# Kernel tuning notes

Measured on AMD Instinct MI355X. Metric: run time of the kernel, lower is better.

## Reference

```python
import jax, jax.numpy as jnp
import numpy as np

V_REST = 0.0
V_RESET = 0.0
V_TH = 1.27
TAU = 50.0
SPIKE_DURATION = 1
SCALE = 100.0  # SurrGradSpike.scale


@jax.custom_vjp
def spike(x):
    return (x > 0).astype(x.dtype)

def _spike_fwd(x):
    return (x > 0).astype(x.dtype), x

def _spike_bwd(x, g):
    # normalized negative part of fast sigmoid (Zenke & Ganguli 2018)
    return (g / (SCALE * jnp.abs(x) + 1.0) ** 2,)

spike.defvjp(_spike_fwd, _spike_bwd)


def _shift(a, k):
    # a[:, j] -> a[:, j + k], zero padded out of range
    if k == 0:
        return a
    if k > 0:
        return jnp.pad(a[:, k:], ((0, 0), (0, k)))
    return jnp.pad(a[:, :k], ((0, 0), (-k, 0)))


def _lif(ode, decay):
    ode2 = ode[..., 0]          # [B, T]
    B, T = ode2.shape
    ode_t = ode2.T              # [T, B] for scan

    def step(carry, inp):
        v, counter, z = carry   # z = remaining steps whose dv reads are zeroed
        t, x = inp
        v = v - decay * (v - V_REST)
        v = jnp.where(counter == 1, V_RESET, v)
        # dv[:, t] was zeroed by a spike within the previous 5 steps (torch in-place window)
        x_eff = jnp.where(z > 0, 0.0, x)
        v = v + x_eff
        v = jnp.where(counter > 1, V_TH, v)
        s = spike(v - V_TH)
        s_d = jax.lax.stop_gradient(s)
        counter = counter + (SPIKE_DURATION + 1) * s_d
        v = jnp.where(counter > 1, V_TH, v)
        # spike at t zeroes dv[:, t-1:t+6]; at t==0 the torch slice [-1:6] is empty
        z = jnp.where((s_d > 0) & (t >= 1), 5.0, jnp.maximum(z - 1.0, 0.0))
        counter = jnp.maximum(counter - 1.0, 0.0)
        return (v, counter, z), (v, s, s_d)

    v0 = jnp.full((B,), V_REST, dtype=ode2.dtype)
    c0 = jnp.zeros((B,), dtype=ode2.dtype)
    z0 = jnp.zeros((B,), dtype=ode2.dtype)
    ts = jnp.arange(T)
    _, (v_rec, s_rec, sd_rec) = jax.lax.scan(step, (v0, c0, z0), (ts, ode_t))
    v_rec = v_rec.T             # [B, T]
    s_rec = s_rec.T             # [B, T]

    sp = sd_rec.T > 0           # detached spike mask [B, T]
    sp = sp.at[:, 0].set(False)  # spike at t=0 zeroes nothing (empty slice in torch)
    # column j of dv is zeroed iff a spike occurred at t' in [j-5, j+1]
    zero_mask = jnp.zeros_like(sp)
    for k in range(-5, 2):
        zero_mask = zero_mask | _shift(sp, k)
    dv = jnp.where(zero_mask, 0.0, ode2)
    return v_rec, s_rec, dv


def setup_inputs() -> dict:
    key = jax.random.key(0)
    B, T = 2048, 4096
    ode = jax.random.normal(key, (B, T, 1), dtype=jnp.float32)
    decay = jnp.float32(1.0 / TAU)  # LIF.decay parameter (learn_tau=False)
    return {"ode": ode, "decay": decay}


def reference(ode, decay):
    return _lif(ode, decay)
```

## Files before the change

kernel.cpp:

```cpp
#include <hip/hip_runtime.h>

constexpr int   T   = 4096;
constexpr float VTH = 1.27f;
constexpr int   K   = 32;
constexpr int   L   = T / K;
constexpr int   LG  = L / 4;
constexpr int   WG  = 160;

__device__ __forceinline__ bool sstep(float x, float decay, float& v, unsigned& h, bool& gate) {
    float t1 = __fmul_rn(decay, v);
    float vd = __fsub_rn(v, t1);
    float xe = gate ? 0.0f : x;
    float vn = __fadd_rn(vd, xe);
    bool  s  = vn > VTH;
    v = s ? 0.0f : vn;
    bool g4 = (h & 15u) != 0u;
    h = (h << 1) | (s ? 1u : 0u);
    gate = s || g4;
    return s;
}

__device__ __forceinline__ bool ostep(float x, float decay, float& v, unsigned& h, bool& gate,
                                      float& vo, float& so, float& dvo, float xprev) {
    float t1 = __fmul_rn(decay, v);
    float vd = __fsub_rn(v, t1);
    float xe = gate ? 0.0f : x;
    float vn = __fadd_rn(vd, xe);
    bool  s  = vn > VTH;
    vo = s ? VTH  : vn;
    so = s ? 1.0f : 0.0f;
    v  = s ? 0.0f : vn;
    bool z6 = s || ((h & 63u) != 0u);
    dvo = z6 ? 0.0f : xprev;
    bool g4 = (h & 15u) != 0u;
    h = (h << 1) | (s ? 1u : 0u);
    gate = s || g4;
    return s;
}

__device__ __forceinline__ void ogroup(float4 X, float decay, float& v, unsigned& h, bool& gate,
                                       float& xprev, float4& vo, float4& so,
                                       float& close, float& px, float& py, float& pz) {
    ostep(X.x, decay, v, h, gate, vo.x, so.x, close, xprev); xprev = X.x;
    ostep(X.y, decay, v, h, gate, vo.y, so.y, px,    xprev); xprev = X.y;
    ostep(X.z, decay, v, h, gate, vo.z, so.z, py,    xprev); xprev = X.z;
    ostep(X.w, decay, v, h, gate, vo.w, so.w, pz,    xprev); xprev = X.w;
}

__device__ __forceinline__ void quad_run(int q, const float4* __restrict__ x4, int g0f,
        float decay, float& v, unsigned& h, bool& gate, float& xprev,
        float4& Xa, float4& Xb, float4& Xc, float4& Xd,
        float4& D0, float4& D1, float4& D2, float4& D3,
        float4& P0, float4& P1, float4& P2, float4& P3,
        float4* __restrict__ v4, float4* __restrict__ s4, float4* __restrict__ d4) {
    float4 V0, V1, V2, V3, S0, S1, S2, S3;
    ogroup(Xa, decay, v, h, gate, xprev, V0, S0, P3.w, D0.x, D0.y, D0.z);
    Xa = x4[g0f + (4*q + 8 < LG ? 4*q + 8 : LG - 1)];
    d4[g0f + 4*q - 4] = P0; d4[g0f + 4*q - 3] = P1;
    d4[g0f + 4*q - 2] = P2; d4[g0f + 4*q - 1] = P3;
    ogroup(Xb, decay, v, h, gate, xprev, V1, S1, D0.w, D1.x, D1.y, D1.z);
    Xb = x4[g0f + (4*q + 9 < LG ? 4*q + 9 : LG - 1)];
    ogroup(Xc, decay, v, h, gate, xprev, V2, S2, D1.w, D2.x, D2.y, D2.z);
    Xc = x4[g0f + (4*q + 10 < LG ? 4*q + 10 : LG - 1)];
    ogroup(Xd, decay, v, h, gate, xprev, V3, S3, D2.w, D3.x, D3.y, D3.z);
    Xd = x4[g0f + (4*q + 11 < LG ? 4*q + 11 : LG - 1)];
    v4[g0f + 4*q] = V0; v4[g0f + 4*q + 1] = V1; v4[g0f + 4*q + 2] = V2; v4[g0f + 4*q + 3] = V3;
    s4[g0f + 4*q] = S0; s4[g0f + 4*q + 1] = S1; s4[g0f + 4*q + 2] = S2; s4[g0f + 4*q + 3] = S3;
}

__global__ __launch_bounds__(64, 1)
void lif_spec(const float* __restrict__ ode, const float* __restrict__ decay_p,
              float* __restrict__ vout, float* __restrict__ sout, float* __restrict__ dvout,
              float2* __restrict__ Sst, float2* __restrict__ Est, int B) {
    const int g = blockIdx.x * 64 + threadIdx.x;
    const int b = g % B;
    const int k = g / B;
    const float decay = decay_p[0];

    const size_t bt = (size_t)b * T;
    const float4* __restrict__ x4 = (const float4*)(ode + bt);
    float4* __restrict__ v4 = (float4*)(vout + bt);
    float4* __restrict__ s4 = (float4*)(sout + bt);
    float4* __restrict__ d4 = (float4*)(dvout + bt);

    const int g0f = k * LG;
    const int wg  = (k == 0) ? 0 : (k * LG < WG ? k * LG : WG);
    float v = 0.0f; unsigned h = 0u; bool gate = false;
    float xprev = 0.0f;

    if (wg > 0) {
        const float4* __restrict__ xw = x4 + (g0f - wg);
        const bool t0row = (g0f - wg == 0);
        float4 Q[16];
#pragma unroll
        for (int i = 0; i < 16; ++i) Q[i] = xw[i];
        for (int c = 0; c < wg; c += 16) {
#pragma unroll
            for (int i = 0; i < 16; ++i) {
                if (i == 0 && c == 0 && t0row) {
                    sstep(Q[0].x, decay, v, h, gate); h = 0u; gate = false;
                    sstep(Q[0].y, decay, v, h, gate);
                    sstep(Q[0].z, decay, v, h, gate);
                    sstep(Q[0].w, decay, v, h, gate);
                } else {
                    sstep(Q[i].x, decay, v, h, gate);
                    sstep(Q[i].y, decay, v, h, gate);
                    sstep(Q[i].z, decay, v, h, gate);
                    sstep(Q[i].w, decay, v, h, gate);
                }
                Q[i] = xw[c + i + 16];
            }
        }
        Sst[k * B + b] = make_float2(v, __uint_as_float(h & 127u));
    }

    float xla = (k < K - 1) ? ode[bt + (size_t)(k + 1) * L] : 0.0f;
    float4 A0 = x4[g0f],     A1 = x4[g0f + 1], A2 = x4[g0f + 2], A3 = x4[g0f + 3];
    float4 B0 = x4[g0f + 4], B1 = x4[g0f + 5], B2 = x4[g0f + 6], B3 = x4[g0f + 7];
    float4 DA0, DA1, DA2, DA3, DB0, DB1, DB2, DB3;

    {
        float4 V0, V1, V2, V3, S0, S1, S2, S3;
        if (k == 0) {
            float dvd;
            bool s0 = ostep(A0.x, decay, v, h, gate, V0.x, S0.x, dvd, xprev); xprev = A0.x;
            h = 0u; gate = false;
            bool s1 = ostep(A0.y, decay, v, h, gate, V0.y, S0.y, DA0.x, xprev); xprev = A0.y;
            ostep(A0.z, decay, v, h, gate, V0.z, S0.z, DA0.y, xprev); xprev = A0.z;
            ostep(A0.w, decay, v, h, gate, V0.w, S0.w, DA0.z, xprev); xprev = A0.w;
            if (s0 && s1) V0.z = VTH;
        } else {
            float cl;
            ogroup(A0, decay, v, h, gate, xprev, V0, S0, cl, DA0.x, DA0.y, DA0.z);
        }
        A0 = x4[g0f + 8];
        ogroup(A1, decay, v, h, gate, xprev, V1, S1, DA0.w, DA1.x, DA1.y, DA1.z); A1 = x4[g0f + 9];
        ogroup(A2, decay, v, h, gate, xprev, V2, S2, DA1.w, DA2.x, DA2.y, DA2.z); A2 = x4[g0f + 10];
        ogroup(A3, decay, v, h, gate, xprev, V3, S3, DA2.w, DA3.x, DA3.y, DA3.z); A3 = x4[g0f + 11];
        v4[g0f] = V0; v4[g0f + 1] = V1; v4[g0f + 2] = V2; v4[g0f + 3] = V3;
        s4[g0f] = S0; s4[g0f + 1] = S1; s4[g0f + 2] = S2; s4[g0f + 3] = S3;
    }

#define MQ(q, Xs, Dn, Pn) quad_run(q, x4, g0f, decay, v, h, gate, xprev, \
        Xs##0, Xs##1, Xs##2, Xs##3, Dn##0, Dn##1, Dn##2, Dn##3, \
        Pn##0, Pn##1, Pn##2, Pn##3, v4, s4, d4);
    MQ(1, B, DB, DA) MQ(2, A, DA, DB) MQ(3, B, DB, DA) MQ(4, A, DA, DB)
    MQ(5, B, DB, DA) MQ(6, A, DA, DB) MQ(7, B, DB, DA)
#undef MQ

    Est[k * B + b] = make_float2(v, __uint_as_float(h & 127u));

    if (k < K - 1) {
        float vo_, so_;
        ostep(xla, decay, v, h, gate, vo_, so_, DB3.w, xprev);
    } else {
        DB3.w = ((h & 63u) != 0u) ? 0.0f : xprev;
    }
    d4[g0f + LG - 4] = DB0; d4[g0f + LG - 3] = DB1;
    d4[g0f + LG - 2] = DB2; d4[g0f + LG - 1] = DB3;
}

__global__ __launch_bounds__(64, 1)
void lif_fix(const float* __restrict__ ode, const float* __restrict__ decay_p,
             float* __restrict__ vout, float* __restrict__ sout, float* __restrict__ dvout,
             const float2* __restrict__ Sst, const float2* __restrict__ Est, int B) {
    const int b = blockIdx.x * 64 + threadIdx.x;
    const float decay = decay_p[0];

    float2 E = Est[b];
    for (int k = 1; k < K; ++k) {
        float2 S = Sst[k * B + b];
        bool match = (S.x == E.x) && (__float_as_uint(S.y) == __float_as_uint(E.y));
        if (match) { E = Est[k * B + b]; continue; }

        const size_t bt = (size_t)b * T;
        const float4* __restrict__ x4 = (const float4*)(ode + bt);
        float4* __restrict__ v4 = (float4*)(vout + bt);
        float4* __restrict__ s4 = (float4*)(sout + bt);
        float4* __restrict__ d4 = (float4*)(dvout + bt);
        const int g0f = k * LG;

        float v = E.x; unsigned h = __float_as_uint(E.y);
        bool gate = (h & 31u) != 0u;
        float xprev = 0.0f;
        float4 pend;

        float4 Q0 = x4[g0f], Q1 = x4[g0f + 1], Q2 = x4[g0f + 2], Q3 = x4[g0f + 3];
        {
            float4 vo, so; float cl;
            ogroup(Q0, decay, v, h, gate, xprev, vo, so, cl, pend.x, pend.y, pend.z);
            v4[g0f] = vo; s4[g0f] = so;
            Q0 = x4[g0f + 4];
        }
#define FPROC(cc, Q) { float4 vo, so; float px, py, pz; \
            ogroup(Q, decay, v, h, gate, xprev, vo, so, pend.w, px, py, pz); \
            d4[g0f + (cc) - 1] = pend; \
            pend.x = px; pend.y = py; pend.z = pz; \
            v4[g0f + (cc)] = vo; s4[g0f + (cc)] = so; }
        FPROC(1, Q1) Q1 = x4[g0f + 5];
        FPROC(2, Q2) Q2 = x4[g0f + 6];
        FPROC(3, Q3) Q3 = x4[g0f + 7];
        for (int c0 = 4; c0 < LG; c0 += 4) {
            FPROC(c0,     Q0) Q0 = x4[g0f + (c0 + 4 < LG ? c0 + 4 : LG - 1)];
            FPROC(c0 + 1, Q1) Q1 = x4[g0f + (c0 + 5 < LG ? c0 + 5 : LG - 1)];
            FPROC(c0 + 2, Q2) Q2 = x4[g0f + (c0 + 6 < LG ? c0 + 6 : LG - 1)];
            FPROC(c0 + 3, Q3) Q3 = x4[g0f + (c0 + 7 < LG ? c0 + 7 : LG - 1)];
        }
#undef FPROC
        E = make_float2(v, __uint_as_float(h & 127u));
        if (k < K - 1) {
            float xla = ode[bt + (size_t)(k + 1) * L];
            float vo_, so_;
            ostep(xla, decay, v, h, gate, vo_, so_, pend.w, xprev);
        } else {
            pend.w = ((h & 63u) != 0u) ? 0.0f : xprev;
        }
        d4[g0f + LG - 1] = pend;
    }
}

extern "C" void kernel_launch(void* const* d_in, const int* in_sizes, int n_in,
                              void* d_out, int out_size, void* d_ws, size_t ws_size,
                              hipStream_t stream) {
    const float* ode   = (const float*)d_in[0];
    const float* decay = (const float*)d_in[1];
    float* out = (float*)d_out;

    const int BT = in_sizes[0];
    const int B  = BT / T;

    float* vout  = out;
    float* sout  = out + (size_t)BT;
    float* dvout = out + 2 * (size_t)BT;

    float2* Sst = (float2*)d_ws;
    float2* Est = Sst + (size_t)K * B;

    lif_spec<<<dim3((B * K) / 64), dim3(64), 0, stream>>>(ode, decay, vout, sout, dvout,
                                                          Sst, Est, B);
    lif_fix<<<dim3(B / 64), dim3(64), 0, stream>>>(ode, decay, vout, sout, dvout,
                                                   Sst, Est, B);
}
```

Baseline: 194.4 us.

## Stage spec-kernel outputs through LDS for coalesced row stores; prefetch fix states

The speculative LIF kernel now buffers each thread's v, spike and dv float4 outputs in shared memory. After each quad of groups a barrier runs, and threads cooperatively write 16-float contiguous chunks spanning 4 rows. This replaces the previous per-thread strided stores, where each lane wrote a different row, so stores become more coalesced. The cost is a barrier per quad and extra LDS traffic. The fix kernel also prefetches the next chunk's start and end states one iteration ahead to hide load latency in its sequential loop.

```diff
diff --git a/kernel.cpp b/kernel.cpp
--- a/kernel.cpp
+++ b/kernel.cpp
@@ -47,41 +47,23 @@
     ostep(X.w, decay, v, h, gate, vo.w, so.w, pz,    xprev); xprev = X.w;
 }
 
-__device__ __forceinline__ void quad_run(int q, const float4* __restrict__ x4, int g0f,
-        float decay, float& v, unsigned& h, bool& gate, float& xprev,
-        float4& Xa, float4& Xb, float4& Xc, float4& Xd,
-        float4& D0, float4& D1, float4& D2, float4& D3,
-        float4& P0, float4& P1, float4& P2, float4& P3,
-        float4* __restrict__ v4, float4* __restrict__ s4, float4* __restrict__ d4) {
-    float4 V0, V1, V2, V3, S0, S1, S2, S3;
-    ogroup(Xa, decay, v, h, gate, xprev, V0, S0, P3.w, D0.x, D0.y, D0.z);
-    Xa = x4[g0f + (4*q + 8 < LG ? 4*q + 8 : LG - 1)];
-    d4[g0f + 4*q - 4] = P0; d4[g0f + 4*q - 3] = P1;
-    d4[g0f + 4*q - 2] = P2; d4[g0f + 4*q - 1] = P3;
-    ogroup(Xb, decay, v, h, gate, xprev, V1, S1, D0.w, D1.x, D1.y, D1.z);
-    Xb = x4[g0f + (4*q + 9 < LG ? 4*q + 9 : LG - 1)];
-    ogroup(Xc, decay, v, h, gate, xprev, V2, S2, D1.w, D2.x, D2.y, D2.z);
-    Xc = x4[g0f + (4*q + 10 < LG ? 4*q + 10 : LG - 1)];
-    ogroup(Xd, decay, v, h, gate, xprev, V3, S3, D2.w, D3.x, D3.y, D3.z);
-    Xd = x4[g0f + (4*q + 11 < LG ? 4*q + 11 : LG - 1)];
-    v4[g0f + 4*q] = V0; v4[g0f + 4*q + 1] = V1; v4[g0f + 4*q + 2] = V2; v4[g0f + 4*q + 3] = V3;
-    s4[g0f + 4*q] = S0; s4[g0f + 4*q + 1] = S1; s4[g0f + 4*q + 2] = S2; s4[g0f + 4*q + 3] = S3;
-}
-
 __global__ __launch_bounds__(64, 1)
 void lif_spec(const float* __restrict__ ode, const float* __restrict__ decay_p,
               float* __restrict__ vout, float* __restrict__ sout, float* __restrict__ dvout,
               float2* __restrict__ Sst, float2* __restrict__ Est, int B) {
-    const int g = blockIdx.x * 64 + threadIdx.x;
-    const int b = g % B;
-    const int k = g / B;
+    __shared__ float4 tv[64 * 5];
+    __shared__ float4 ts[64 * 5];
+    __shared__ float4 td[2][64 * 5];
+
+    const int tid = threadIdx.x;
+    const int gg  = blockIdx.x * 64;
+    const int rb  = gg % B;
+    const int k   = gg / B;
+    const int b   = rb + tid;
     const float decay = decay_p[0];
 
     const size_t bt = (size_t)b * T;
     const float4* __restrict__ x4 = (const float4*)(ode + bt);
-    float4* __restrict__ v4 = (float4*)(vout + bt);
-    float4* __restrict__ s4 = (float4*)(sout + bt);
-    float4* __restrict__ d4 = (float4*)(dvout + bt);
 
     const int g0f = k * LG;
     const int wg  = (k == 0) ? 0 : (k * LG < WG ? k * LG : WG);
@@ -114,50 +96,91 @@
         Sst[k * B + b] = make_float2(v, __uint_as_float(h & 127u));
     }
 
+    int rowoff0 = (rb + (tid >> 2)) * T + k * L + (tid & 3) * 4;
+    const int wbase = tid * 5;
+    const int rbase = (tid >> 2) * 5 + (tid & 3);
+
     float xla = (k < K - 1) ? ode[bt + (size_t)(k + 1) * L] : 0.0f;
     float4 A0 = x4[g0f],     A1 = x4[g0f + 1], A2 = x4[g0f + 2], A3 = x4[g0f + 3];
     float4 B0 = x4[g0f + 4], B1 = x4[g0f + 5], B2 = x4[g0f + 6], B3 = x4[g0f + 7];
-    float4 DA0, DA1, DA2, DA3, DB0, DB1, DB2, DB3;
+    float4 Pd;
+
+#define OG(X, gidx) { float4 V_, S_; float cl_, p0_, p1_, p2_; \
+        ogroup(X, decay, v, h, gate, xprev, V_, S_, cl_, p0_, p1_, p2_); \
+        if ((gidx) > 0) { Pd.w = cl_; td[(((gidx)-1) >> 2) & 1][wbase + (((gidx)-1) & 3)] = Pd; } \
+        Pd.x = p0_; Pd.y = p1_; Pd.z = p2_; \
+        tv[wbase + ((gidx) & 3)] = V_; ts[wbase + ((gidx) & 3)] = S_; }
+
+#define FLUSH(q) { __syncthreads(); \
+        float4 Vv0 = tv[rbase], Vv1 = tv[rbase + 80], Vv2 = tv[rbase + 160], Vv3 = tv[rbase + 240]; \
+        float4 Ss0 = ts[rbase], Ss1 = ts[rbase + 80], Ss2 = ts[rbase + 160], Ss3 = ts[rbase + 240]; \
+        *(float4*)(vout + rowoff0 + (q)*16)            = Vv0; \
+        *(float4*)(vout + rowoff0 + 16*T + (q)*16)     = Vv1; \
+        *(float4*)(vout + rowoff0 + 32*T + (q)*16)     = Vv2; \
+        *(float4*)(vout + rowoff0 + 48*T + (q)*16)     = Vv3; \
+        *(float4*)(sout + rowoff0 + (q)*16)            = Ss0; \
+        *(float4*)(sout + rowoff0 + 16*T + (q)*16)     = Ss1; \
+        *(float4*)(sout + rowoff0 + 32*T + (q)*16)     = Ss2; \
+        *(float4*)(sout + rowoff0 + 48*T + (q)*16)     = Ss3; \
+        if ((q) >= 1) { \
+            float4 Dd0 = td[((q)-1)&1][rbase],       Dd1 = td[((q)-1)&1][rbase + 80]; \
+            float4 Dd2 = td[((q)-1)&1][rbase + 160], Dd3 = td[((q)-1)&1][rbase + 240]; \
+            *(float4*)(dvout + rowoff0 + ((q)-1)*16)        = Dd0; \
+            *(float4*)(dvout + rowoff0 + 16*T + ((q)-1)*16) = Dd1; \
+            *(float4*)(dvout + rowoff0 + 32*T + ((q)-1)*16) = Dd2; \
+            *(float4*)(dvout + rowoff0 + 48*T + ((q)-1)*16) = Dd3; } }
 
     {
-        float4 V0, V1, V2, V3, S0, S1, S2, S3;
         if (k == 0) {
-            float dvd;
-            bool s0 = ostep(A0.x, decay, v, h, gate, V0.x, S0.x, dvd, xprev); xprev = A0.x;
+            float4 V_, S_; float dvd;
+            bool s0 = ostep(A0.x, decay, v, h, gate, V_.x, S_.x, dvd, xprev); xprev = A0.x;
             h = 0u; gate = false;
-            bool s1 = ostep(A0.y, decay, v, h, gate, V0.y, S0.y, DA0.x, xprev); xprev = A0.y;
-            ostep(A0.z, decay, v, h, gate, V0.z, S0.z, DA0.y, xprev); xprev = A0.z;
-            ostep(A0.w, decay, v, h, gate, V0.w, S0.w, DA0.z, xprev); xprev = A0.w;
-            if (s0 && s1) V0.z = VTH;
+            bool s1 = ostep(A0.y, decay, v, h, gate, V_.y, S_.y, Pd.x, xprev); xprev = A0.y;
+            ostep(A0.z, decay, v, h, gate, V_.z, S_.z, Pd.y, xprev); xprev = A0.z;
+            ostep(A0.w, decay, v, h, gate, V_.w, S_.w, Pd.z, xprev); xprev = A0.w;
+            if (s0 && s1) V_.z = VTH;
+            tv[wbase] = V_; ts[wbase] = S_;
         } else {
-            float cl;
-            ogroup(A0, decay, v, h, gate, xprev, V0, S0, cl, DA0.x, DA0.y, DA0.z);
+            float4 V_, S_; float cl_;
+            ogroup(A0, decay, v, h, gate, xprev, V_, S_, cl_, Pd.x, Pd.y, Pd.z);
+            tv[wbase] = V_; ts[wbase] = S_;
         }
         A0 = x4[g0f + 8];
-        ogroup(A1, decay, v, h, gate, xprev, V1, S1, DA0.w, DA1.x, DA1.y, DA1.z); A1 = x4[g0f + 9];
-        ogroup(A2, decay, v, h, gate, xprev, V2, S2, DA1.w, DA2.x, DA2.y, DA2.z); A2 = x4[g0f + 10];
-        ogroup(A3, decay, v, h, gate, xprev, V3, S3, DA2.w, DA3.x, DA3.y, DA3.z); A3 = x4[g0f + 11];
-        v4[g0f] = V0; v4[g0f + 1] = V1; v4[g0f + 2] = V2; v4[g0f + 3] = V3;
-        s4[g0f] = S0; s4[g0f + 1] = S1; s4[g0f + 2] = S2; s4[g0f + 3] = S3;
-    }
-
-#define MQ(q, Xs, Dn, Pn) quad_run(q, x4, g0f, decay, v, h, gate, xprev, \
-        Xs##0, Xs##1, Xs##2, Xs##3, Dn##0, Dn##1, Dn##2, Dn##3, \
-        Pn##0, Pn##1, Pn##2, Pn##3, v4, s4, d4);
-    MQ(1, B, DB, DA) MQ(2, A, DA, DB) MQ(3, B, DB, DA) MQ(4, A, DA, DB)
-    MQ(5, B, DB, DA) MQ(6, A, DA, DB) MQ(7, B, DB, DA)
+        OG(A1, 1) A1 = x4[g0f + 9];
+        OG(A2, 2) A2 = x4[g0f + 10];
+        OG(A3, 3) A3 = x4[g0f + 11];
+        FLUSH(0)
+    }
+
+#define MQ(q, Xs) \
+        OG(Xs##0, 4*(q)+0) Xs##0 = x4[g0f + (4*(q)+8  < LG ? 4*(q)+8  : LG-1)]; \
+        OG(Xs##1, 4*(q)+1) Xs##1 = x4[g0f + (4*(q)+9  < LG ? 4*(q)+9  : LG-1)]; \
+        OG(Xs##2, 4*(q)+2) Xs##2 = x4[g0f + (4*(q)+10 < LG ? 4*(q)+10 : LG-1)]; \
+        OG(Xs##3, 4*(q)+3) Xs##3 = x4[g0f + (4*(q)+11 < LG ? 4*(q)+11 : LG-1)]; \
+        FLUSH(q)
+    MQ(1, B) MQ(2, A) MQ(3, B) MQ(4, A) MQ(5, B) MQ(6, A) MQ(7, B)
 #undef MQ
+#undef OG
 
     Est[k * B + b] = make_float2(v, __uint_as_float(h & 127u));
 
     if (k < K - 1) {
         float vo_, so_;
-        ostep(xla, decay, v, h, gate, vo_, so_, DB3.w, xprev);
+        ostep(xla, decay, v, h, gate, vo_, so_, Pd.w, xprev);
     } else {
-        DB3.w = ((h & 63u) != 0u) ? 0.0f : xprev;
-    }
-    d4[g0f + LG - 4] = DB0; d4[g0f + LG - 3] = DB1;
-    d4[g0f + LG - 2] = DB2; d4[g0f + LG - 1] = DB3;
+        Pd.w = ((h & 63u) != 0u) ? 0.0f : xprev;
+    }
+    td[1][wbase + 3] = Pd;
+    __syncthreads();
+    {
+        float4 Dd0 = td[1][rbase],       Dd1 = td[1][rbase + 80];
+        float4 Dd2 = td[1][rbase + 160], Dd3 = td[1][rbase + 240];
+        *(float4*)(dvout + rowoff0 + 7*16)        = Dd0;
+        *(float4*)(dvout + rowoff0 + 16*T + 7*16) = Dd1;
+        *(float4*)(dvout + rowoff0 + 32*T + 7*16) = Dd2;
+        *(float4*)(dvout + rowoff0 + 48*T + 7*16) = Dd3;
+    }
+#undef FLUSH
 }
 
 __global__ __launch_bounds__(64, 1)
@@ -167,11 +190,14 @@
     const int b = blockIdx.x * 64 + threadIdx.x;
     const float decay = decay_p[0];
 
-    float2 E = Est[b];
+    float2 E  = Est[b];
+    float2 S1 = Sst[B + b];
+    float2 E1 = Est[B + b];
     for (int k = 1; k < K; ++k) {
-        float2 S = Sst[k * B + b];
+        float2 S = S1, Ek = E1;
+        if (k + 1 < K) { S1 = Sst[(k + 1) * B + b]; E1 = Est[(k + 1) * B + b]; }
         bool match = (S.x == E.x) && (__float_as_uint(S.y) == __float_as_uint(E.y));
-        if (match) { E = Est[k * B + b]; continue; }
+        if (match) { E = Ek; continue; }
 
         const size_t bt = (size_t)b * T;
         const float4* __restrict__ x4 = (const float4*)(ode + bt);
```

Result: faster. 180.1 us (-7.3%).
